# Kernel optimization log

Measured on AMD Instinct MI355X. Metric: run time of the kernel, lower is better.

## Reference

```python
import jax, jax.numpy as jnp
import numpy as np

D_MODEL = 1024
N_HEADS = 16
D_K = D_MODEL // N_HEADS


def setup_inputs() -> dict:
    key = jax.random.key(0)
    ks = jax.random.split(key, 7)
    s = 1.0 / np.sqrt(D_MODEL)
    return {
        "x": jax.random.normal(ks[0], (2, 2048, D_MODEL), dtype=jnp.float32),
        "w_q": jax.random.uniform(ks[1], (D_MODEL, D_MODEL), jnp.float32, -s, s),
        "w_k": jax.random.uniform(ks[2], (D_MODEL, D_MODEL), jnp.float32, -s, s),
        "w_v": jax.random.uniform(ks[3], (D_MODEL, D_MODEL), jnp.float32, -s, s),
        "w_o": jax.random.uniform(ks[4], (D_MODEL, D_MODEL), jnp.float32, -s, s),
        "b_o": jax.random.uniform(ks[5], (D_MODEL,), jnp.float32, -s, s),
        "ln_gamma": jnp.ones((D_MODEL,), jnp.float32),
        "ln_beta": jnp.zeros((D_MODEL,), jnp.float32),
    }


def reference(x, w_q, w_k, w_v, w_o, b_o, ln_gamma, ln_beta):
    # Pre-LN
    mu = jnp.mean(x, axis=-1, keepdims=True)
    var = jnp.mean(jnp.square(x - mu), axis=-1, keepdims=True)
    x_norm = (x - mu) / jnp.sqrt(var + 1e-5) * ln_gamma + ln_beta

    B, S, _ = x.shape
    # torch Linear: y = x @ W.T ; weights stored [out, in]
    def proj(w):
        return (x_norm @ w.T).reshape(B, S, N_HEADS, D_K).transpose(0, 2, 1, 3)

    Q, K, V = proj(w_q), proj(w_k), proj(w_v)  # [B,H,S,Dk]
    scores = jnp.einsum("bhqd,bhkd->bhqk", Q, K) / np.sqrt(D_K)
    attn = jax.nn.softmax(scores, axis=-1)
    attended = jnp.einsum("bhqk,bhkd->bhqd", attn, V)
    attended = attended.transpose(0, 2, 1, 3).reshape(B, S, D_MODEL)
    out = attended @ w_o.T + b_o
    return x + out
```

## Files before the change

### kernel.cpp

```cpp
#include <hip/hip_runtime.h>

typedef _Float16 f16;
typedef _Float16 f16x8 __attribute__((ext_vector_type(8)));
typedef _Float16 f16x4 __attribute__((ext_vector_type(4)));
typedef _Float16 f16x2 __attribute__((ext_vector_type(2)));
typedef __fp16 fp16x2 __attribute__((ext_vector_type(2)));
typedef float f32x4 __attribute__((ext_vector_type(4)));

#define SEQ   2048
#define DM    1024
#define DKH   64
#define MTOT  4096

__device__ __forceinline__ f32x4 mfma16(f16x8 a, f16x8 b, f32x4 c) {
  return __builtin_amdgcn_mfma_f32_16x16x32_f16(a, b, c, 0, 0, 0);
}

__device__ __forceinline__ f16x2 cvt_pk(float a, float b) {
  fp16x2 r = __builtin_amdgcn_cvt_pkrtz(a, b);
  return __builtin_bit_cast(f16x2, r);
}

__device__ __forceinline__ void gload16(const f16* g, f16* l) {
  __builtin_amdgcn_global_load_lds(
      (const __attribute__((address_space(1))) void*)g,
      (__attribute__((address_space(3))) void*)l, 16, 0, 0);
}

__global__ __launch_bounds__(256) void cast_all(const float* __restrict__ w_q,
                                                const float* __restrict__ w_k,
                                                const float* __restrict__ w_v,
                                                const float* __restrict__ w_o,
                                                f16* __restrict__ out) {
  const int sel = blockIdx.x >> 10;
  const float* src = sel == 0 ? w_q : sel == 1 ? w_k : sel == 2 ? w_v : w_o;
  const int i = ((blockIdx.x & 1023) * 256 + threadIdx.x) * 4;
  float4 v = *reinterpret_cast<const float4*>(src + i);
  f16x4 o;
  o[0] = (f16)v.x; o[1] = (f16)v.y; o[2] = (f16)v.z; o[3] = (f16)v.w;
  *reinterpret_cast<f16x4*>(out + (size_t)sel * 1048576 + i) = o;
}

__global__ __launch_bounds__(256) void ln_kernel(const float* __restrict__ x,
                                                 const float* __restrict__ gamma,
                                                 const float* __restrict__ beta,
                                                 f16* __restrict__ xn) {
  const int row = blockIdx.x, t = threadIdx.x;
  const float* xr = x + (size_t)row * DM;
  float v[4], s = 0.f, s2 = 0.f;
#pragma unroll
  for (int i = 0; i < 4; ++i) {
    v[i] = xr[t + i * 256];
    s += v[i];
    s2 += v[i] * v[i];
  }
#pragma unroll
  for (int o = 32; o > 0; o >>= 1) {
    s  += __shfl_down(s, o);
    s2 += __shfl_down(s2, o);
  }
  __shared__ float ps[4], ps2[4], mu_s, rs_s;
  if ((t & 63) == 0) { ps[t >> 6] = s; ps2[t >> 6] = s2; }
  __syncthreads();
  if (t == 0) {
    float a = ps[0] + ps[1] + ps[2] + ps[3];
    float b = ps2[0] + ps2[1] + ps2[2] + ps2[3];
    float mu = a * (1.f / DM);
    float var = b * (1.f / DM) - mu * mu;
    mu_s = mu;
    rs_s = rsqrtf(var + 1e-5f);
  }
  __syncthreads();
  const float mu = mu_s, rs = rs_s;
#pragma unroll
  for (int i = 0; i < 4; ++i) {
    int d = t + i * 256;
    xn[(size_t)row * DM + d] = (f16)(((v[i] - mu) * rs) * gamma[d] + beta[d]);
  }
}

__global__ __launch_bounds__(256) void gemm_qkv(const f16* __restrict__ A,
                                                const f16* __restrict__ Wqkv,
                                                f16* __restrict__ qb,
                                                f16* __restrict__ kb,
                                                f16* __restrict__ vtb) {
  __shared__ f16 sA[128][64];
  __shared__ f16 sB[64][64];
  const int t = threadIdx.x, l = t & 63, w = t >> 6;
  const int wr = w >> 1, wc = w & 1, lg = l >> 4, lm = l & 15;
  const int m0 = blockIdx.y * 128, n0 = blockIdx.x * 64;
  const int crow = l >> 3;
  const int scol = ((l & 7) ^ crow) << 3;
  const int rsw  = (lm & 7) << 3;

  f32x4 acc[4][2] = {};

  for (int k0 = 0; k0 < DM; k0 += 64) {
    __syncthreads();
#pragma unroll
    for (int cc = 0; cc < 4; ++cc) {
      const int c = w + cc * 4;
      gload16(A + (size_t)(m0 + c * 8 + crow) * DM + k0 + scol, &sA[c * 8][0]);
    }
#pragma unroll
    for (int cc = 0; cc < 2; ++cc) {
      const int c = w + cc * 4;
      gload16(Wqkv + (size_t)(n0 + c * 8 + crow) * DM + k0 + scol, &sB[c * 8][0]);
    }
    __syncthreads();
#pragma unroll
    for (int kk = 0; kk < 2; ++kk) {
      f16x8 af[4], bf[2];
#pragma unroll
      for (int i = 0; i < 4; ++i)
        af[i] = *(const f16x8*)&sA[wr * 64 + i * 16 + lm][(kk * 32 + lg * 8) ^ rsw];
#pragma unroll
      for (int i = 0; i < 2; ++i)
        bf[i] = *(const f16x8*)&sB[wc * 32 + i * 16 + lm][(kk * 32 + lg * 8) ^ rsw];
#pragma unroll
      for (int mi = 0; mi < 4; ++mi)
#pragma unroll
        for (int ni = 0; ni < 2; ++ni)
          acc[mi][ni] = mfma16(af[mi], bf[ni], acc[mi][ni]);
    }
  }

  const int sel = blockIdx.x >> 4;
  if (sel < 2) {
    f16* outp = sel == 0 ? qb : kb;
    const int nloc = n0 - sel * 1024;
#pragma unroll
    for (int mi = 0; mi < 4; ++mi) {
      const int rowb = m0 + wr * 64 + mi * 16 + lg * 4;
#pragma unroll
      for (int ni = 0; ni < 2; ++ni) {
        const int col = nloc + wc * 32 + ni * 16 + lm;
#pragma unroll
        for (int r = 0; r < 4; ++r)
          outp[(size_t)(rowb + r) * DM + col] = (f16)acc[mi][ni][r];
      }
    }
  } else {
#pragma unroll
    for (int mi = 0; mi < 4; ++mi) {
      const int rowb = m0 + wr * 64 + mi * 16 + lg * 4;
      const int b = rowb >> 11, s = rowb & 2047;
#pragma unroll
      for (int ni = 0; ni < 2; ++ni) {
        const int col = (n0 - 2048) + wc * 32 + ni * 16 + lm;
        f16x4 o;
        o[0] = (f16)acc[mi][ni][0]; o[1] = (f16)acc[mi][ni][1];
        o[2] = (f16)acc[mi][ni][2]; o[3] = (f16)acc[mi][ni][3];
        *reinterpret_cast<f16x4*>(&vtb[(size_t)(b * 1024 + col) * SEQ + s]) = o;
      }
    }
  }
}

__global__ __launch_bounds__(256) void gemm_out(const f16* __restrict__ A,
                                                const f16* __restrict__ W,
                                                float* __restrict__ out,
                                                const float* __restrict__ bias,
                                                const float* __restrict__ resid) {
  __shared__ f16 sA[64][64];
  __shared__ f16 sB[128][64];
  const int t = threadIdx.x, l = t & 63, w = t >> 6;
  const int wr = w >> 1, wc = w & 1, lg = l >> 4, lm = l & 15;
  const int m0 = blockIdx.y * 64, n0 = blockIdx.x * 128;
  const int crow = l >> 3;
  const int scol = ((l & 7) ^ crow) << 3;
  const int rsw  = (lm & 7) << 3;

  f32x4 acc[2][4] = {};

  for (int k0 = 0; k0 < DM; k0 += 64) {
    __syncthreads();
#pragma unroll
    for (int cc = 0; cc < 2; ++cc) {
      const int c = w + cc * 4;
      gload16(A + (size_t)(m0 + c * 8 + crow) * DM + k0 + scol, &sA[c * 8][0]);
    }
#pragma unroll
    for (int cc = 0; cc < 4; ++cc) {
      const int c = w + cc * 4;
      gload16(W + (size_t)(n0 + c * 8 + crow) * DM + k0 + scol, &sB[c * 8][0]);
    }
    __syncthreads();
#pragma unroll
    for (int kk = 0; kk < 2; ++kk) {
      f16x8 af[2], bf[4];
#pragma unroll
      for (int i = 0; i < 2; ++i)
        af[i] = *(const f16x8*)&sA[wr * 32 + i * 16 + lm][(kk * 32 + lg * 8) ^ rsw];
#pragma unroll
      for (int i = 0; i < 4; ++i)
        bf[i] = *(const f16x8*)&sB[wc * 64 + i * 16 + lm][(kk * 32 + lg * 8) ^ rsw];
#pragma unroll
      for (int mi = 0; mi < 2; ++mi)
#pragma unroll
        for (int ni = 0; ni < 4; ++ni)
          acc[mi][ni] = mfma16(af[mi], bf[ni], acc[mi][ni]);
    }
  }

#pragma unroll
  for (int mi = 0; mi < 2; ++mi) {
    const int rowb = m0 + wr * 32 + mi * 16 + lg * 4;
#pragma unroll
    for (int ni = 0; ni < 4; ++ni) {
      const int col = n0 + wc * 64 + ni * 16 + lm;
#pragma unroll
      for (int r = 0; r < 4; ++r) {
        const size_t idx = (size_t)(rowb + r) * DM + col;
        out[idx] = resid[idx] + bias[col] + acc[mi][ni][r];
      }
    }
  }
}

__global__ __launch_bounds__(256) void attn_kernel(const f16* __restrict__ Qb,
                                                   const f16* __restrict__ Kb,
                                                   const f16* __restrict__ Vt,
                                                   f16* __restrict__ Ob) {
  __shared__ f16 sK[2][64][64];
  __shared__ f16 sV[2][64][64];

  int bx = blockIdx.x;
  bx = (bx & 7) * 64 + (bx >> 3);
  const int qt = bx & 15, bh = bx >> 4;
  const int h = bh & 15, b = bh >> 4;
  const int t = threadIdx.x, l = t & 63, w = t >> 6;
  const int lg = l >> 4, lm = l & 15;
  const float K2 = 0.18033688f;

  f16x8 qf[2][2];
#pragma unroll
  for (int qg = 0; qg < 2; ++qg) {
    const f16* qptr =
        Qb + (size_t)(b * SEQ + qt * 128 + w * 32 + qg * 16 + lm) * DM + h * DKH;
    qf[qg][0] = *(const f16x8*)(qptr + lg * 8);
    qf[qg][1] = *(const f16x8*)(qptr + 32 + lg * 8);
#pragma unroll
    for (int j = 0; j < 8; ++j) {
      qf[qg][0][j] = (f16)((float)qf[qg][0][j] * K2);
      qf[qg][1][j] = (f16)((float)qf[qg][1][j] * K2);
    }
  }

  const f16x8 ones = {(f16)1, (f16)1, (f16)1, (f16)1,
                      (f16)1, (f16)1, (f16)1, (f16)1};

  f32x4 oacc[2][4] = {};
  f32x4 oden[2] = {};

  const int crow = l >> 3;
  const int scol = ((l & 7) ^ crow) << 3;
  const int rsw  = (lm & 7) << 3;

  auto stage = [&](int buf, int kt) {
#pragma unroll
    for (int cc = 0; cc < 2; ++cc) {
      const int c = w + cc * 4;
      const int row = c * 8 + crow;
      const int nfp = row >> 4, lgp = (row >> 2) & 3, rp = row & 3;
      const int key = (nfp >> 1) * 32 + lgp * 8 + (nfp & 1) * 4 + rp;
      gload16(Kb + (size_t)(b * SEQ + kt * 64 + key) * DM + h * DKH + scol,
              &sK[buf][c * 8][0]);
      gload16(Vt + (size_t)(bh * DKH + row) * SEQ + kt * 64 + scol,
              &sV[buf][c * 8][0]);
    }
  };

  stage(0, 0);
  __syncthreads();
  int cur = 0;

  for (int kt = 0; kt < SEQ / 64; ++kt) {
    if (kt < SEQ / 64 - 1) stage(cur ^ 1, kt + 1);

    f32x4 sc[2][4] = {};
    __builtin_amdgcn_s_setprio(1);
#pragma unroll
    for (int kk = 0; kk < 2; ++kk)
#pragma unroll
      for (int nf = 0; nf < 4; ++nf) {
        f16x8 kf = *(const f16x8*)&sK[cur][nf * 16 + lm][(kk * 32 + lg * 8) ^ rsw];
        sc[0][nf] = mfma16(kf, qf[0][kk], sc[0][nf]);
        sc[1][nf] = mfma16(kf, qf[1][kk], sc[1][nf]);
      }
    __builtin_amdgcn_s_setprio(0);

    union PU { f16x8 v; f16x2 h[4]; };
    PU pu[2][2];
#pragma unroll
    for (int qg = 0; qg < 2; ++qg)
#pragma unroll
      for (int nf = 0; nf < 4; ++nf) {
        float e0 = __builtin_amdgcn_exp2f(sc[qg][nf][0]);
        float e1 = __builtin_amdgcn_exp2f(sc[qg][nf][1]);
        float e2 = __builtin_amdgcn_exp2f(sc[qg][nf][2]);
        float e3 = __builtin_amdgcn_exp2f(sc[qg][nf][3]);
        pu[qg][nf >> 1].h[(nf & 1) * 2 + 0] = cvt_pk(e0, e1);
        pu[qg][nf >> 1].h[(nf & 1) * 2 + 1] = cvt_pk(e2, e3);
      }

    __builtin_amdgcn_s_setprio(1);
#pragma unroll
    for (int ks = 0; ks < 2; ++ks) {
#pragma unroll
      for (int ni = 0; ni < 4; ++ni) {
        f16x8 vf = *(const f16x8*)&sV[cur][ni * 16 + lm][(ks * 32 + lg * 8) ^ rsw];
        oacc[0][ni] = mfma16(pu[0][ks].v, vf, oacc[0][ni]);
        oacc[1][ni] = mfma16(pu[1][ks].v, vf, oacc[1][ni]);
      }
      oden[0] = mfma16(pu[0][ks].v, ones, oden[0]);
      oden[1] = mfma16(pu[1][ks].v, ones, oden[1]);
    }
    __builtin_amdgcn_s_setprio(0);

    __syncthreads();
    cur ^= 1;
  }

#pragma unroll
  for (int qg = 0; qg < 2; ++qg) {
    float rd[4];
#pragma unroll
    for (int r = 0; r < 4; ++r) rd[r] = 1.f / oden[qg][r];
#pragma unroll
    for (int ni = 0; ni < 4; ++ni)
#pragma unroll
      for (int r = 0; r < 4; ++r) {
        const int q = qt * 128 + w * 32 + qg * 16 + lg * 4 + r;
        const int d = ni * 16 + lm;
        Ob[(size_t)(b * SEQ + q) * DM + h * DKH + d] = (f16)(oacc[qg][ni][r] * rd[r]);
      }
  }
}

extern "C" void kernel_launch(void* const* d_in, const int* in_sizes, int n_in,
                              void* d_out, int out_size, void* d_ws, size_t ws_size,
                              hipStream_t stream) {
  const float* x   = (const float*)d_in[0];
  const float* w_q = (const float*)d_in[1];
  const float* w_k = (const float*)d_in[2];
  const float* w_v = (const float*)d_in[3];
  const float* w_o = (const float*)d_in[4];
  const float* b_o = (const float*)d_in[5];
  const float* lng = (const float*)d_in[6];
  const float* lnb = (const float*)d_in[7];
  float* out = (float*)d_out;

  char* ws = (char*)d_ws;
  const size_t MB = 1ull << 20;
  f16* xn   = (f16*)(ws + 0 * MB);
  f16* wqkv = (f16*)(ws + 8 * MB);
  f16* woh  = (f16*)(ws + 14 * MB);
  f16* qb   = (f16*)(ws + 16 * MB);
  f16* kb   = (f16*)(ws + 24 * MB);
  f16* vtb  = (f16*)(ws + 32 * MB);
  f16* att  = (f16*)(ws + 40 * MB);

  cast_all<<<4096, 256, 0, stream>>>(w_q, w_k, w_v, w_o, wqkv);
  ln_kernel<<<MTOT, 256, 0, stream>>>(x, lng, lnb, xn);

  gemm_qkv<<<dim3(48, 32), 256, 0, stream>>>(xn, wqkv, qb, kb, vtb);
  attn_kernel<<<512, 256, 0, stream>>>(qb, kb, vtb, att);
  gemm_out<<<dim3(8, 64), 256, 0, stream>>>(att, woh, out, b_o, x);
}
```

Measured before the change: 121.3 us.

## Merge weight cast with layernorm and double attention key tile to 128

The weight-cast and layernorm kernels are merged into one prep launch, dropping one kernel launch. The attention kernel now stages 128 keys per iteration instead of 64, with precomputed, incrementing global pointers and a new V swizzle. This halves the number of barriers and staging rounds in the key loop. The cost is twice the LDS per block, which may lower occupancy.

Result: faster. 116.4 us (-4.1%).

```diff
diff --git a/kernel.cpp b/kernel.cpp
--- a/kernel.cpp
+++ b/kernel.cpp
@@ -27,25 +27,27 @@
       (__attribute__((address_space(3))) void*)l, 16, 0, 0);
 }
 
-__global__ __launch_bounds__(256) void cast_all(const float* __restrict__ w_q,
-                                                const float* __restrict__ w_k,
-                                                const float* __restrict__ w_v,
-                                                const float* __restrict__ w_o,
-                                                f16* __restrict__ out) {
-  const int sel = blockIdx.x >> 10;
-  const float* src = sel == 0 ? w_q : sel == 1 ? w_k : sel == 2 ? w_v : w_o;
-  const int i = ((blockIdx.x & 1023) * 256 + threadIdx.x) * 4;
-  float4 v = *reinterpret_cast<const float4*>(src + i);
-  f16x4 o;
-  o[0] = (f16)v.x; o[1] = (f16)v.y; o[2] = (f16)v.z; o[3] = (f16)v.w;
-  *reinterpret_cast<f16x4*>(out + (size_t)sel * 1048576 + i) = o;
-}
-
-__global__ __launch_bounds__(256) void ln_kernel(const float* __restrict__ x,
-                                                 const float* __restrict__ gamma,
-                                                 const float* __restrict__ beta,
-                                                 f16* __restrict__ xn) {
-  const int row = blockIdx.x, t = threadIdx.x;
+__global__ __launch_bounds__(256) void prep_kernel(const float* __restrict__ x,
+                                                   const float* __restrict__ w_q,
+                                                   const float* __restrict__ w_k,
+                                                   const float* __restrict__ w_v,
+                                                   const float* __restrict__ w_o,
+                                                   const float* __restrict__ gamma,
+                                                   const float* __restrict__ beta,
+                                                   f16* __restrict__ wout,
+                                                   f16* __restrict__ xn) {
+  const int t = threadIdx.x;
+  if (blockIdx.x < 4096) {
+    const int sel = blockIdx.x >> 10;
+    const float* src = sel == 0 ? w_q : sel == 1 ? w_k : sel == 2 ? w_v : w_o;
+    const int i = ((blockIdx.x & 1023) * 256 + t) * 4;
+    float4 v = *reinterpret_cast<const float4*>(src + i);
+    f16x4 o;
+    o[0] = (f16)v.x; o[1] = (f16)v.y; o[2] = (f16)v.z; o[3] = (f16)v.w;
+    *reinterpret_cast<f16x4*>(wout + (size_t)sel * 1048576 + i) = o;
+    return;
+  }
+  const int row = blockIdx.x - 4096;
   const float* xr = x + (size_t)row * DM;
   float v[4], s = 0.f, s2 = 0.f;
 #pragma unroll
@@ -222,8 +224,8 @@
                                                    const f16* __restrict__ Kb,
                                                    const f16* __restrict__ Vt,
                                                    f16* __restrict__ Ob) {
-  __shared__ f16 sK[2][64][64];
-  __shared__ f16 sV[2][64][64];
+  __shared__ f16 sK[2][128][64];
+  __shared__ f16 sV[2][64][128];
 
   int bx = blockIdx.x;
   bx = (bx & 7) * 64 + (bx >> 3);
@@ -257,66 +259,83 @@
   const int scol = ((l & 7) ^ crow) << 3;
   const int rsw  = (lm & 7) << 3;
 
-  auto stage = [&](int buf, int kt) {
-#pragma unroll
-    for (int cc = 0; cc < 2; ++cc) {
-      const int c = w + cc * 4;
-      const int row = c * 8 + crow;
-      const int nfp = row >> 4, lgp = (row >> 2) & 3, rp = row & 3;
-      const int key = (nfp >> 1) * 32 + lgp * 8 + (nfp & 1) * 4 + rp;
-      gload16(Kb + (size_t)(b * SEQ + kt * 64 + key) * DM + h * DKH + scol,
-              &sK[buf][c * 8][0]);
-      gload16(Vt + (size_t)(bh * DKH + row) * SEQ + kt * 64 + scol,
-              &sV[buf][c * 8][0]);
+  const f16* kptr[4];
+  const f16* vptr[4];
+#pragma unroll
+  for (int cc = 0; cc < 4; ++cc) {
+    const int ck = w + cc * 4;
+    const int krow = ck * 8 + crow;
+    const int half = krow >> 6, r6 = krow & 63;
+    const int nfp = r6 >> 4, lgp = (r6 >> 2) & 3, rp = r6 & 3;
+    const int key = half * 64 + (nfp >> 1) * 32 + lgp * 8 + (nfp & 1) * 4 + rp;
+    kptr[cc] = Kb + (size_t)(b * SEQ + key) * DM + h * DKH + scol;
+    const int drow = ck * 4 + (l >> 4);
+    const int vcol = ((l & 15) ^ ((ck & 1) * 4 + (l >> 4))) << 3;
+    vptr[cc] = Vt + (size_t)(bh * DKH + drow) * SEQ + vcol;
+  }
+
+  auto stage = [&](int buf) {
+#pragma unroll
+    for (int cc = 0; cc < 4; ++cc) {
+      const int ck = w + cc * 4;
+      gload16(kptr[cc], &sK[buf][ck * 8][0]);
+      gload16(vptr[cc], &sV[buf][ck * 4][0]);
+      kptr[cc] += 128 * DM;
+      vptr[cc] += 128;
     }
   };
 
-  stage(0, 0);
+  stage(0);
   __syncthreads();
   int cur = 0;
 
-  for (int kt = 0; kt < SEQ / 64; ++kt) {
-    if (kt < SEQ / 64 - 1) stage(cur ^ 1, kt + 1);
-
-    f32x4 sc[2][4] = {};
-    __builtin_amdgcn_s_setprio(1);
-#pragma unroll
-    for (int kk = 0; kk < 2; ++kk)
-#pragma unroll
-      for (int nf = 0; nf < 4; ++nf) {
-        f16x8 kf = *(const f16x8*)&sK[cur][nf * 16 + lm][(kk * 32 + lg * 8) ^ rsw];
-        sc[0][nf] = mfma16(kf, qf[0][kk], sc[0][nf]);
-        sc[1][nf] = mfma16(kf, qf[1][kk], sc[1][nf]);
-      }
-    __builtin_amdgcn_s_setprio(0);
-
-    union PU { f16x8 v; f16x2 h[4]; };
-    PU pu[2][2];
-#pragma unroll
-    for (int qg = 0; qg < 2; ++qg)
-#pragma unroll
-      for (int nf = 0; nf < 4; ++nf) {
-        float e0 = __builtin_amdgcn_exp2f(sc[qg][nf][0]);
-        float e1 = __builtin_amdgcn_exp2f(sc[qg][nf][1]);
-        float e2 = __builtin_amdgcn_exp2f(sc[qg][nf][2]);
-        float e3 = __builtin_amdgcn_exp2f(sc[qg][nf][3]);
-        pu[qg][nf >> 1].h[(nf & 1) * 2 + 0] = cvt_pk(e0, e1);
-        pu[qg][nf >> 1].h[(nf & 1) * 2 + 1] = cvt_pk(e2, e3);
-      }
-
-    __builtin_amdgcn_s_setprio(1);
-#pragma unroll
-    for (int ks = 0; ks < 2; ++ks) {
-#pragma unroll
-      for (int ni = 0; ni < 4; ++ni) {
-        f16x8 vf = *(const f16x8*)&sV[cur][ni * 16 + lm][(ks * 32 + lg * 8) ^ rsw];
-        oacc[0][ni] = mfma16(pu[0][ks].v, vf, oacc[0][ni]);
-        oacc[1][ni] = mfma16(pu[1][ks].v, vf, oacc[1][ni]);
-      }
-      oden[0] = mfma16(pu[0][ks].v, ones, oden[0]);
-      oden[1] = mfma16(pu[1][ks].v, ones, oden[1]);
-    }
-    __builtin_amdgcn_s_setprio(0);
+  for (int kt = 0; kt < SEQ / 128; ++kt) {
+    if (kt < SEQ / 128 - 1) stage(cur ^ 1);
+
+#pragma unroll
+    for (int half = 0; half < 2; ++half) {
+      f32x4 sc[2][4] = {};
+      __builtin_amdgcn_s_setprio(1);
+#pragma unroll
+      for (int kk = 0; kk < 2; ++kk)
+#pragma unroll
+        for (int nf = 0; nf < 4; ++nf) {
+          f16x8 kf = *(const f16x8*)
+              &sK[cur][half * 64 + nf * 16 + lm][(kk * 32 + lg * 8) ^ rsw];
+          sc[0][nf] = mfma16(kf, qf[0][kk], sc[0][nf]);
+          sc[1][nf] = mfma16(kf, qf[1][kk], sc[1][nf]);
+        }
+      __builtin_amdgcn_s_setprio(0);
+
+      union PU { f16x8 v; f16x2 hh[4]; };
+      PU pu[2][2];
+#pragma unroll
+      for (int qg = 0; qg < 2; ++qg)
+#pragma unroll
+        for (int nf = 0; nf < 4; ++nf) {
+          float e0 = __builtin_amdgcn_exp2f(sc[qg][nf][0]);
+          float e1 = __builtin_amdgcn_exp2f(sc[qg][nf][1]);
+          float e2 = __builtin_amdgcn_exp2f(sc[qg][nf][2]);
+          float e3 = __builtin_amdgcn_exp2f(sc[qg][nf][3]);
+          pu[qg][nf >> 1].hh[(nf & 1) * 2 + 0] = cvt_pk(e0, e1);
+          pu[qg][nf >> 1].hh[(nf & 1) * 2 + 1] = cvt_pk(e2, e3);
+        }
+
+      __builtin_amdgcn_s_setprio(1);
+#pragma unroll
+      for (int ks = 0; ks < 2; ++ks) {
+#pragma unroll
+        for (int ni = 0; ni < 4; ++ni) {
+          f16x8 vf = *(const f16x8*)
+              &sV[cur][ni * 16 + lm][(half * 64 + ks * 32 + lg * 8) ^ rsw];
+          oacc[0][ni] = mfma16(pu[0][ks].v, vf, oacc[0][ni]);
+          oacc[1][ni] = mfma16(pu[1][ks].v, vf, oacc[1][ni]);
+        }
+        oden[0] = mfma16(pu[0][ks].v, ones, oden[0]);
+        oden[1] = mfma16(pu[1][ks].v, ones, oden[1]);
+      }
+      __builtin_amdgcn_s_setprio(0);
+    }
 
     __syncthreads();
     cur ^= 1;
@@ -361,9 +380,7 @@
   f16* vtb  = (f16*)(ws + 32 * MB);
   f16* att  = (f16*)(ws + 40 * MB);
 
-  cast_all<<<4096, 256, 0, stream>>>(w_q, w_k, w_v, w_o, wqkv);
-  ln_kernel<<<MTOT, 256, 0, stream>>>(x, lng, lnb, xn);
-
+  prep_kernel<<<8192, 256, 0, stream>>>(x, w_q, w_k, w_v, w_o, lng, lnb, wqkv, xn);
   gemm_qkv<<<dim3(48, 32), 256, 0, stream>>>(xn, wqkv, qb, kb, vtb);
   attn_kernel<<<512, 256, 0, stream>>>(qb, kb, vtb, att);
   gemm_out<<<dim3(8, 64), 256, 0, stream>>>(att, woh, out, b_o, x);
```
